# Kernel tuning notes

Hardware: AMD Instinct MI355X
Metric: run time of the kernel (lower is better)

Reference implementation:

```python
import jax, jax.numpy as jnp
import numpy as np
from jax import lax

B, T, H, M, K, Q, P = 32, 128, 256, 1000, 3, 4, 2  # batch, phones, hidden, max_mel_len, kernel, q_out, p_out


def _ln(x, g, b, eps=1e-5):
    mu = jnp.mean(x, -1, keepdims=True)
    var = jnp.mean((x - mu) ** 2, -1, keepdims=True)
    return (x - mu) * lax.rsqrt(var + eps) * g + b


def _forward(x, x_mask, x_dur, params):
    (proj_w, proj_b, conv_w, conv_b, conv_g, conv_beta,
     q_w1, q_b1, q_g, q_beta, q_w2, q_b2,
     p_w1, p_b1, p_g, p_beta, p_w2, p_b2,
     proj1_w, proj1_b, proj2_w, proj2_b, projo_w, projo_b) = params

    valid = (~x_mask).astype(x.dtype)[:, :, None]                      # (B,T,1), 1 = real phone
    # proj -> ConvBlock (shared between the w and c branches; dropout is identity in eval)
    h = x @ proj_w + proj_b                                            # (B,T,H)
    hc = lax.conv_general_dilated((h * valid).transpose(0, 2, 1), conv_w,
                                  (1,), 'SAME',
                                  dimension_numbers=('NCH', 'OIH', 'NCH'))
    hc = hc.transpose(0, 2, 1) + conv_b                                # (B,T,8)
    hc = jax.nn.silu(_ln(hc, conv_g, conv_beta)) * valid               # (B,T,8)

    mel_lens = jnp.minimum(jnp.round(jnp.sum(x_dur, -1)).astype(jnp.int32), M)
    mel_pad = jnp.arange(M)[None, :] >= mel_lens[:, None]              # (B,M) True = padded frame
    mask = x_mask[:, None, :] | mel_pad[:, :, None]                    # (B,M,T)

    e = jnp.cumsum(x_dur, -1)                                          # phone end times
    s = e - x_dur                                                      # phone start times
    t = jnp.arange(1, M + 1, dtype=x.dtype)
    E = jnp.where(mask, 0.0, e[:, None, :] - t[None, :, None])         # (B,M,T)
    S = jnp.where(mask, 0.0, t[None, :, None] - s[:, None, :])         # (B,M,T)

    feat = jnp.concatenate([jnp.broadcast_to(hc[:, None], (B, M, T, 8)),
                            S[..., None], E[..., None]], axis=-1)      # (B,M,T,10)

    # mlp_q scores -> masked softmax over phone axis
    sc = jax.nn.silu(_ln(feat @ q_w1 + q_b1, q_g, q_beta)) @ q_w2 + q_b2   # (B,M,T,Q)
    sc = jnp.where(x_mask[:, None, :, None], -jnp.inf, sc)
    w = jax.nn.softmax(sc, axis=2)
    w = jnp.where(mel_pad[:, :, None, None], 0.0, w)                   # (B,M,T,Q)

    # mlp_p per-(frame,phone) auxiliary features
    c = jax.nn.silu(_ln(feat @ p_w1 + p_b1, p_g, p_beta)) @ p_w2 + p_b2    # (B,M,T,P)

    # dual einsum combine (matches torch permute+view ordering: q-major then feature)
    wh = jnp.einsum('bmnq,bnh->bmqh', w, x).reshape(B, M, Q * H) @ proj1_w + proj1_b
    wc = jnp.einsum('bmnq,bmnp->bmqp', w, c).reshape(B, M, Q * P) @ proj2_w + proj2_b
    o = jnp.where(mel_pad[:, :, None], 0.0, wh + wc) @ projo_w + projo_b   # (B,M,2H)

    mel_mask = jnp.broadcast_to(mel_pad[:, :, None], (B, M, T))
    return o, mel_mask, mel_lens, jnp.transpose(w, (0, 3, 1, 2))


def setup_inputs() -> dict:
    key = jax.random.key(0)
    ks = jax.random.split(key, 16)
    x = jax.random.normal(ks[0], (B, T, H), jnp.float32)
    x_lengths = jax.random.randint(ks[1], (B,), T // 2, T + 1).at[0].set(T)
    x_mask = jnp.arange(T)[None, :] >= x_lengths[:, None]              # True = pad
    x_dur = jax.random.uniform(ks[2], (B, T), jnp.float32, 2.0, 10.0)
    x_dur = x_dur * (~x_mask)
    x_dur = x_dur.at[0].multiply(2.0)  # element 0 total duration > M -> static max_mel_len = M

    def xavier(k, shape):
        return jax.random.normal(k, shape, jnp.float32) * jnp.sqrt(2.0 / (shape[0] + shape[1]))

    return dict(
        x=x, x_mask=x_mask, x_dur=x_dur, x_lengths=x_lengths,
        proj_w=xavier(ks[3], (H, H)), proj_b=jnp.zeros((H,)),
        conv_w=jax.random.normal(ks[4], (8, H, K), jnp.float32) * 0.05, conv_b=jnp.zeros((8,)),
        conv_g=jnp.ones((8,)), conv_beta=jnp.zeros((8,)),
        q_w1=xavier(ks[5], (10, Q)), q_b1=jnp.zeros((Q,)),
        q_g=jnp.ones((Q,)), q_beta=jnp.zeros((Q,)),
        q_w2=xavier(ks[6], (Q, Q)), q_b2=jnp.zeros((Q,)),
        p_w1=xavier(ks[7], (10, P)), p_b1=jnp.zeros((P,)),
        p_g=jnp.ones((P,)), p_beta=jnp.zeros((P,)),
        p_w2=xavier(ks[8], (P, P)), p_b2=jnp.zeros((P,)),
        proj1_w=xavier(ks[9], (H * Q, H)), proj1_b=jnp.zeros((H,)),
        proj2_w=xavier(ks[10], (Q * P, H)), proj2_b=jnp.zeros((H,)),
        projo_w=xavier(ks[11], (H, 2 * H)), projo_b=jnp.zeros((2 * H,)),
    )


def reference(x, x_mask, x_dur, x_lengths,
              proj_w, proj_b, conv_w, conv_b, conv_g, conv_beta,
              q_w1, q_b1, q_g, q_beta, q_w2, q_b2,
              p_w1, p_b1, p_g, p_beta, p_w2, p_b2,
              proj1_w, proj1_b, proj2_w, proj2_b, projo_w, projo_b):
    params = (proj_w, proj_b, conv_w, conv_b, conv_g, conv_beta,
              q_w1, q_b1, q_g, q_beta, q_w2, q_b2,
              p_w1, p_b1, p_g, p_beta, p_w2, p_b2,
              proj1_w, proj1_b, proj2_w, proj2_b, projo_w, projo_b)
    return _forward(x, x_mask, x_dur, params)
```

## Files before the change

kernel.cpp:

```cpp
#include <hip/hip_runtime.h>
#include <math.h>

#define BB 32
#define TT 128
#define HH 256
#define MM 1000

typedef __attribute__((ext_vector_type(8))) short short8;
typedef __attribute__((ext_vector_type(4))) float floatx4;

__device__ inline void fma4(float4& a, const float4 b, float s) {
    a.x += b.x * s; a.y += b.y * s; a.z += b.z * s; a.w += b.w * s;
}

__device__ inline unsigned short f2bf(float f) {
    union { float f; unsigned int u; } c; c.f = f;
    unsigned int u = c.u;
    return (unsigned short)((u + 0x7FFFu + ((u >> 16) & 1u)) >> 16);
}

__device__ inline float bf2f(unsigned short h) {
    union { unsigned int u; float f; } c; c.u = ((unsigned int)h) << 16; return c.f;
}


__global__ __launch_bounds__(256) void kF1(
    const float* __restrict__ x, const float* __restrict__ pw_h_,
    const float* __restrict__ pb_h, float* __restrict__ h,
    const float* __restrict__ p1w, const float* __restrict__ po,
    float* __restrict__ PWpart,
    unsigned short* __restrict__ xh, unsigned short* __restrict__ xl,
    const float* __restrict__ dur, float* __restrict__ e_cum,
    int* __restrict__ ml_i, float* __restrict__ ml_out,
    unsigned short* __restrict__ w_bf) {
    __shared__ __align__(16) float S1[4096];
    int gb = blockIdx.x;
    int tid = threadIdx.x;

    if (gb < 256) {
        float (*xs)[HH] = (float(*)[HH])S1;
        int b = gb >> 3, tt = gb & 7;
        int t0 = tt * 16;
        for (int e = tid; e < 16 * HH; e += 256) {
            int r = e >> 8, i = e & 255;
            xs[r][i] = x[(b * TT + t0 + r) * HH + i];
        }
        __syncthreads();
        int jg = tid & 63, rg = tid >> 6;
        int j4 = jg * 4;
        float4 bias = *(const float4*)(pb_h + j4);
        float4 acc[4];
        #pragma unroll
        for (int ri = 0; ri < 4; ++ri) acc[ri] = bias;
        #pragma unroll 4
        for (int i = 0; i < HH; ++i) {
            float4 wv = *(const float4*)(pw_h_ + i * HH + j4);
            #pragma unroll
// ... 38 lines not shown
        #pragma unroll
        for (int k = 0; k < 4; ++k) {
            unsigned short hv = f2bf(vv[k]);
            hi.us[k] = hv;
            lo.us[k] = f2bf(vv[k] - bf2f(hv));
        }
        *(uint2*)(xh + idx) = hi.u;
        *(uint2*)(xl + idx) = lo.u;
    } else {
        int b = gb - 1792;
        if (tid < 64) {
            #pragma unroll
            for (int q = 0; q < 4; ++q) {
                uint4* dst = (uint4*)(w_bf + (((size_t)(b * 4 + q)) * 1024 + 1000) * 128);
                for (int e = tid; e < 384; e += 64) dst[e] = make_uint4(0, 0, 0, 0);
            }
            if (tid == 0) {
                float run = 0.f;
                const float* d = dur + b * TT;
                float* e = e_cum + b * TT;
                for (int t = 0; t < TT; ++t) { run += d[t]; e[t] = run; }
                int ml = (int)rintf(run);
                if (ml > MM) ml = MM;
                if (ml < 0) ml = 0;
                ml_i[b] = ml;
                ml_out[b] = (float)ml;
            }
        }
    }
}

__global__ __launch_bounds__(256) void kF2(
    const float* __restrict__ h, const float* __restrict__ cw,
    const int* __restrict__ xlen, float* __restrict__ hcpre,
    const float* __restrict__ PWpart,
    unsigned short* __restrict__ pwh, unsigned short* __restrict__ pwl,
    const float* __restrict__ p2w, const float* __restrict__ po,
    const float* __restrict__ p1b, const float* __restrict__ p2b,
    const float* __restrict__ pob,
    float* __restrict__ P2o, float* __restrict__ bvec) {
    __shared__ __align__(16) float S2[10778];
    int gb = blockIdx.x;
    int tid = threadIdx.x;

    if (gb < 256) {
        float (*hs)[257] = (float(*)[257])S2;
        float (*cws)[769] = (float(*)[769])(S2 + 4626);
        int b = gb >> 3, tt = gb & 7;
        int t0 = tt * 16;
        int L = xlen[b];
        for (int e = tid; e < 18 * 256; e += 256) {
            int r = e >> 8, i = e & 255;
            int t = t0 - 1 + r;
            float v = 0.f;
            if (t >= 0 && t < TT && t < L) v = h[((size_t)b * TT + t) * HH + i];
            hs[r][i] = v;
        }
        for (int e = tid; e < 6144; e += 256) {
            int o = e / 768, rem = e - o * 768;
            cws[o][rem] = cw[e];
        }
        __syncthreads();
        if (tid < 128) {
            int o = tid >> 4, tl = tid & 15;
            float acc = 0.f;
            #pragma unroll
            for (int k = 0; k < 3; ++k) {
                const float* wr = &cws[o][k];
                const float* hr = hs[tl + k];
                #pragma unroll 8
                for (int i = 0; i < 256; ++i) acc += hr[i] * wr[i * 3];
            }
            hcpre[((size_t)b * TT + t0 + tl) * 8 + o] = acc;
        }
    } else if (gb < 384) {
        float (*S)[65] = (float(*)[65])S2;
        int blk = gb - 256;
        int nt = blk & 31, ct = blk >> 5;
        int c0 = ct * 64, n0 = nt * 64;
        for (int e = tid; e < 4096; e += 256) {
            int cc = e >> 6, nn = e & 63;
            size_t off = (size_t)(c0 + cc) * 2048 + n0 + nn;
            float v = PWpart[off] + PWpart[524288 + off]
                    + PWpart[2 * 524288 + off] + PWpart[3 * 524288 + off];
            S[cc][nn] = v;
        }
        __syncthreads();
        for (int e = tid; e < 4096; e += 256) {
            int nn = e >> 6, cc = e & 63;
            float v = S[cc][nn];
            unsigned short hv = f2bf(v);
            size_t d = (size_t)(n0 + nn) * 256 + c0 + cc;
            pwh[d] = hv;
            pwl[d] = f2bf(v - bf2f(hv));
        }
    } else {
        for (int j = tid; j < 512; j += 256) {
            float acc[9];
            #pragma unroll
            for (int r = 0; r < 9; ++r) acc[r] = 0.f;
            for (int c = 0; c < HH; ++c) {
                float pv = po[c * 512 + j];
                #pragma unroll
                for (int r = 0; r < 8; ++r) acc[r] += p2w[r * HH + c] * pv;
                acc[8] += (p1b[c] + p2b[c]) * pv;
            }
            #pragma unroll
            for (int r = 0; r < 8; ++r) P2o[r * 512 + j] = acc[r];
            bvec[j] = acc[8] + pob[j];
        }
    }
}

__device__ inline int swzk(int row, int chunk) {
    return row * 32 + ((chunk ^ ((row >> 1) & 3)) << 3);
}

__global__ __launch_bounds__(256) void kF3(
    const unsigned short* __restrict__ xh, const unsigned short* __restrict__ xl,
    const unsigned short* __restrict__ pwh, const unsigned short* __restrict__ pwl,
    unsigned short* __restrict__ A2T,
    const float* __restrict__ hcpre, const float* __restrict__ cb,
    const float* __restrict__ cg, const float* __restrict__ cbeta,
    const float* __restrict__ qw1, const float* __restrict__ qb1,
    const float* __restrict__ pw1, const float* __restrict__ pb1,
    const float* __restrict__ e_cum, const float* __restrict__ dur,
    const int* __restrict__ xlen,
    float* __restrict__ baseq, float* __restrict__ basep) {
    __shared__ __align__(16) unsigned short SM[16384];
    int gblk = blockIdx.x;
    int tid = threadIdx.x;

    if (gblk >= 512) {
        int b = gblk - 512;
        int t = tid;
        if (t < 128) {
            int L = xlen[b];
            float v[8];
            float mu = 0.f;
            #pragma unroll
            for (int o = 0; o < 8; ++o) { v[o] = hcpre[(b * TT + t) * 8 + o] + cb[o]; mu += v[o]; }
            mu *= 0.125f;
            float var = 0.f;
            #pragma unroll
            for (int o = 0; o < 8; ++o) { float d = v[o] - mu; var += d * d; }
            var *= 0.125f;
            float rs = 1.0f / sqrtf(var + 1e-5f);
            float valid = (t < L) ? 1.f : 0.f;
            #pragma unroll
            for (int o = 0; o < 8; ++o) {
                float a = (v[o] - mu) * rs * cg[o] + cbeta[o];
                v[o] = a / (1.f + expf(-a)) * valid;
            }
            float e = e_cum[b * TT + t];
            float s_ = e - dur[b * TT + t];
            #pragma unroll
            for (int j = 0; j < 4; ++j) {
                float acc = qb1[j];
                #pragma unroll
                for (int o = 0; o < 8; ++o) acc += v[o] * qw1[o * 4 + j];
                acc += e * qw1[9 * 4 + j] - s_ * qw1[8 * 4 + j];
                baseq[(b * TT + t) * 4 + j] = acc;
            }
            #pragma unroll
            for (int j = 0; j < 2; ++j) {
                float acc = pb1[j];
                #pragma unroll
                for (int o = 0; o < 8; ++o) acc += v[o] * pw1[o * 2 + j];
                acc += e * pw1[9 * 2 + j] - s_ * pw1[8 * 2 + j];
                basep[(b * TT + t) * 2 + j] = acc;
            }
        }
        return;
    }

    unsigned short* Ah = SM;
    unsigned short* Al = SM + 4096;
    unsigned short* Bh = SM + 8192;
    unsigned short* Bl = SM + 12288;
    int blk = gblk;
    int b = blk >> 4, nt = blk & 15;
    int n0 = nt * 128;
    int lane = tid & 63, wv = tid >> 6;
    int wm = wv & 1, wn = wv >> 1;

    floatx4 acc[16];
    #pragma unroll
    for (int i = 0; i < 16; ++i) acc[i] = (floatx4){0.f, 0.f, 0.f, 0.f};

    int srow = tid >> 1, shalf = tid & 1;
    const unsigned short* gxh = xh + ((size_t)(b * TT + srow) * 256 + shalf * 16);
    const unsigned short* gxl = xl + ((size_t)(b * TT + srow) * 256 + shalf * 16);
    const unsigned short* gph = pwh + ((size_t)(n0 + srow) * 256 + shalf * 16);
    const unsigned short* gpl = pwl + ((size_t)(n0 + srow) * 256 + shalf * 16);
    int wAd0 = swzk(srow, 2 * shalf);
    int wAd1 = swzk(srow, 2 * shalf + 1);

    int ra = wm * 64 + (lane & 15);
    int rb = wn * 64 + (lane & 15);
    int cq = lane >> 4;

    for (int kc = 0; kc < 256; kc += 32) {
        uint4 a0 = *(const uint4*)(gxh + kc);
        uint4 a1 = *(const uint4*)(gxh + kc + 8);
// ... 18 lines not shown
        }
        #pragma unroll
        for (int i = 0; i < 4; ++i)
            #pragma unroll
            for (int j = 0; j < 4; ++j) {
                floatx4 c = acc[i * 4 + j];
                c = __builtin_amdgcn_mfma_f32_16x16x32_bf16(afh[i], bfh[j], c, 0, 0, 0);
                c = __builtin_amdgcn_mfma_f32_16x16x32_bf16(afh[i], bfl[j], c, 0, 0, 0);
                c = __builtin_amdgcn_mfma_f32_16x16x32_bf16(afl[i], bfh[j], c, 0, 0, 0);
                acc[i * 4 + j] = c;
            }
        __syncthreads();
    }

    unsigned short* OT = SM;
    #pragma unroll
    for (int i = 0; i < 4; ++i)
        #pragma unroll
        for (int j = 0; j < 4; ++j) {
            int nloc = wn * 64 + j * 16 + (lane & 15);
            int tb = wm * 64 + i * 16 + ((lane >> 4) << 2);
            union { unsigned short us[4]; uint2 v; } pk;
            #pragma unroll
            for (int r = 0; r < 4; ++r) pk.us[r] = f2bf(acc[i * 4 + j][r]);
            int chunk = tb >> 3, sub = tb & 7;
            *(uint2*)&OT[nloc * 128 + (((chunk ^ (nloc & 15)) << 3) | sub)] = pk.v;
        }
    __syncthreads();
    int q = n0 >> 9, jb = n0 & 511;
    for (int u = tid; u < 2048; u += 256) {
        int nrow = u >> 4, seg = u & 15;
        uint4 v = *(const uint4*)&OT[nrow * 128 + ((seg ^ (nrow & 15)) << 3)];
        *(uint4*)(A2T + (((size_t)(b * 4 + q) * 512) + jb + nrow) * 128 + seg * 8) = v;
    }
}

__global__ __launch_bounds__(256) void k_wsoft(
    const float* __restrict__ baseq, const float* __restrict__ basep,
    const float* __restrict__ qw1, const float* __restrict__ qg,
    const float* __restrict__ qbeta, const float* __restrict__ qw2,
    const float* __restrict__ qb2,
    const float* __restrict__ pw1, const float* __restrict__ pg,
    const float* __restrict__ pbeta, const float* __restrict__ pw2,
    const float* __restrict__ pb2,
    const int* __restrict__ xlen, const int* __restrict__ ml_i,
    float* __restrict__ w_out, float* __restrict__ mm_out,
    float* __restrict__ wc8, unsigned short* __restrict__ w_bf) {
    int blk = blockIdx.x;
    int b = blk / 250;
    int mg = blk - b * 250;
    int wv = threadIdx.x >> 6, lane = threadIdx.x & 63;
    int m = mg * 4 + wv;
    int ml = ml_i[b];
    int t1 = lane, t2 = lane + 64;
    bool pad = (m >= ml);
    size_t mmbase = ((size_t)b * MM + m) * TT;
    mm_out[mmbase + t1] = pad ? 1.f : 0.f;
    mm_out[mmbase + t2] = pad ? 1.f : 0.f;
    if (pad) {
        #pragma unroll
        for (int q = 0; q < 4; ++q) {
            size_t wb = ((size_t)(b * 4 + q) * MM + m) * TT;
            w_out[wb + t1] = 0.f;
            w_out[wb + t2] = 0.f;
            unsigned short* wbq = w_bf + (((size_t)(b * 4 + q)) * 1024 + m) * 128;
            wbq[t1] = 0; wbq[t2] = 0;
        }
        if (lane == 0) {
            #pragma unroll
            for (int r = 0; r < 8; ++r) wc8[((size_t)b * MM + m) * 8 + r] = 0.f;
        }
        return;
    }
    int L = xlen[b];
    float mp1 = (float)(m + 1);
    float dq[4];
    #pragma unroll
    for (int j = 0; j < 4; ++j) dq[j] = mp1 * (qw1[8 * 4 + j] - qw1[9 * 4 + j]);

    float sc1[4], sc2[4];
    float c1v[2], c2v[2];
    #pragma unroll
    for (int half = 0; half < 2; ++half) {
        int t = half ? t2 : t1;
        float* sc = half ? sc2 : sc1;
        float* cv = half ? c2v : c1v;
        if (t < L) {
            float4 bq = *(const float4*)(baseq + ((size_t)b * TT + t) * 4);
            float z[4] = {bq.x + dq[0], bq.y + dq[1], bq.z + dq[2], bq.w + dq[3]};
            float mu = 0.25f * (z[0] + z[1] + z[2] + z[3]);
            float var = 0.f;
            #pragma unroll
            for (int j = 0; j < 4; ++j) { float d = z[j] - mu; var += d * d; }
            var *= 0.25f;
            float rs = 1.f / sqrtf(var + 1e-5f);
            float a[4];
            #pragma unroll
            for (int j = 0; j < 4; ++j) {
                float av = (z[j] - mu) * rs * qg[j] + qbeta[j];
                a[j] = av / (1.f + expf(-av));
            }
            #pragma unroll
            for (int q = 0; q < 4; ++q) {
                float s = qb2[q];
                #pragma unroll
                for (int j = 0; j < 4; ++j) s += a[j] * qw2[j * 4 + q];
                sc[q] = s;
            }
            float z0 = basep[((size_t)b * TT + t) * 2 + 0] + mp1 * (pw1[16] - pw1[18]);
            float z1 = basep[((size_t)b * TT + t) * 2 + 1] + mp1 * (pw1[17] - pw1[19]);
            float pmu = 0.5f * (z0 + z1);
            float d0 = z0 - pmu, d1 = z1 - pmu;
            float pvar = 0.5f * (d0 * d0 + d1 * d1);
            float prs = 1.f / sqrtf(pvar + 1e-5f);
            float a0 = d0 * prs * pg[0] + pbeta[0];
            float a1 = d1 * prs * pg[1] + pbeta[1];
            a0 = a0 / (1.f + expf(-a0));
            a1 = a1 / (1.f + expf(-a1));
            cv[0] = pb2[0] + a0 * pw2[0] + a1 * pw2[2];
            cv[1] = pb2[1] + a0 * pw2[1] + a1 * pw2[3];
        } else {
            sc[0] = sc[1] = sc[2] = sc[3] = -__builtin_inff();
            cv[0] = cv[1] = 0.f;
        }
    }
    float w1[4], w2[4];
    #pragma unroll
    for (int q = 0; q < 4; ++q) {
        float mx = fmaxf(sc1[q], sc2[q]);
        #pragma unroll
        for (int off = 32; off > 0; off >>= 1) mx = fmaxf(mx, __shfl_xor(mx, off, 64));
        float e1 = expf(sc1[q] - mx);
        float e2 = expf(sc2[q] - mx);
        float s = e1 + e2;
        #pragma unroll
        for (int off = 32; off > 0; off >>= 1) s += __shfl_xor(s, off, 64);
        w1[q] = e1 / s;
        w2[q] = e2 / s;
        size_t wb = ((size_t)(b * 4 + q) * MM + m) * TT;
        w_out[wb + t1] = w1[q];
        w_out[wb + t2] = w2[q];
        unsigned short* wbq = w_bf + (((size_t)(b * 4 + q)) * 1024 + m) * 128;
        wbq[t1] = f2bf(w1[q]);
        wbq[t2] = f2bf(w2[q]);
    }
    float red[8];
    #pragma unroll
    for (int r8 = 0; r8 < 8; ++r8) {
        int q = r8 >> 1, p = r8 & 1;
        float v = w1[q] * c1v[p] + w2[q] * c2v[p];
        #pragma unroll
        for (int off = 32; off > 0; off >>= 1) v += __shfl_xor(v, off, 64);
        red[r8] = v;
    }
    if (lane == 0) {
        #pragma unroll
        for (int r8 = 0; r8 < 8; ++r8) wc8[((size_t)b * MM + m) * 8 + r8] = red[r8];
    }
}

__global__ __launch_bounds__(256, 2) void k_main(
    const unsigned short* __restrict__ w_bf, const unsigned short* __restrict__ A2T,
    const float* __restrict__ wc8, const float* __restrict__ P2o,
    const float* __restrict__ bvec, const float* __restrict__ pob,
    const int* __restrict__ ml_i, float* __restrict__ o_out) {
    __shared__ __align__(16) unsigned short Asm[2][128 * 40];
    __shared__ __align__(16) unsigned short Bsm[2][128 * 40];
    int wgid = blockIdx.x;
    int blk = (wgid & 7) * 128 + (wgid >> 3);
    int nt = blk & 3, mt = (blk >> 2) & 7, b = blk >> 5;
    int m0 = mt * 128, n0 = nt * 128;
    int tid = threadIdx.x;
    int ml = ml_i[b];

    if (m0 >= ml) {
        float* pb_s = (float*)&Asm[0][0];
        if (tid < 128) pb_s[tid] = pob[n0 + tid];
        __syncthreads();
        int col4 = (tid & 31) * 4;
        float4 pv = *(const float4*)&pb_s[col4];
        for (int r = tid >> 5; r < 128; r += 8) {
            int m = m0 + r;
            if (m < MM)
                *(float4*)(o_out + ((size_t)b * MM + m) * 512 + n0 + col4) = pv;
        }
        return;
    }

    int lane = tid & 63, wv = tid >> 6;
    int wm = wv & 1, wn = wv >> 1;
// ... 109 lines not shown
                              void* d_out, int out_size, void* d_ws, size_t ws_size,
                              hipStream_t stream) {
    (void)in_sizes; (void)n_in; (void)out_size; (void)ws_size;
    const float* x      = (const float*)d_in[0];
    const float* dur    = (const float*)d_in[2];
    const int*   xlen   = (const int*)d_in[3];
    const float* proj_w = (const float*)d_in[4];
    const float* proj_b = (const float*)d_in[5];
    const float* conv_w = (const float*)d_in[6];
    const float* conv_b = (const float*)d_in[7];
    const float* conv_g = (const float*)d_in[8];
    const float* conv_be= (const float*)d_in[9];
    const float* q_w1   = (const float*)d_in[10];
    const float* q_b1   = (const float*)d_in[11];
    const float* q_g    = (const float*)d_in[12];
    const float* q_be   = (const float*)d_in[13];
    const float* q_w2   = (const float*)d_in[14];
    const float* q_b2   = (const float*)d_in[15];
    const float* p_w1   = (const float*)d_in[16];
    const float* p_b1   = (const float*)d_in[17];
    const float* p_g    = (const float*)d_in[18];
    const float* p_be   = (const float*)d_in[19];
    const float* p_w2   = (const float*)d_in[20];
    const float* p_b2   = (const float*)d_in[21];
    const float* p1w    = (const float*)d_in[22];
    const float* p1b    = (const float*)d_in[23];
    const float* p2w    = (const float*)d_in[24];
    const float* p2b    = (const float*)d_in[25];
    const float* pow_   = (const float*)d_in[26];
    const float* pob    = (const float*)d_in[27];

    float* ws    = (float*)d_ws;
    float* e_cum = ws + 0;
    float* hcpre = ws + 4096;
    float* baseq = ws + 36864;
    float* basep = ws + 53248;
    float* h     = ws + 61440;
    unsigned short* pw_h = (unsigned short*)(ws + 1110016);
    unsigned short* pw_l = (unsigned short*)(ws + 1372160);
    unsigned short* A2T = (unsigned short*)(ws + 1634304);
    float* wc8   = ws + 5828608;
    float* P2o   = ws + 6084608;
    float* bvec  = ws + 6088704;
    int*   ml_i  = (int*)(ws + 6089216);
    float* PWpart= ws + 6090752;
    unsigned short* w_bf = (unsigned short*)(ws + 8187904);
    unsigned short* x_hi = (unsigned short*)(ws + 16576512);
    unsigned short* x_lo = (unsigned short*)(ws + 17100800);

    float* o_out  = (float*)d_out;
    float* mm_out = o_out + 16384000;
    float* ml_out = o_out + 20480000;
    float* w_out  = o_out + 20480032;

    kF1<<<dim3(1824), dim3(256), 0, stream>>>(x, proj_w, proj_b, h,
                                              p1w, pow_, PWpart,
                                              x_hi, x_lo,
                                              dur, e_cum, ml_i, ml_out, w_bf);
    kF2<<<dim3(385), dim3(256), 0, stream>>>(h, conv_w, xlen, hcpre,
                                             PWpart, pw_h, pw_l,
                                             p2w, pow_, p1b, p2b, pob, P2o, bvec);
    kF3<<<dim3(544), dim3(256), 0, stream>>>(x_hi, x_lo, pw_h, pw_l, A2T,
                                             hcpre, conv_b, conv_g, conv_be,
                                             q_w1, q_b1, p_w1, p_b1,
                                             e_cum, dur, xlen, baseq, basep);
    k_wsoft<<<dim3(BB * 250), dim3(256), 0, stream>>>(baseq, basep,
                                                      q_w1, q_g, q_be, q_w2, q_b2,
                                                      p_w1, p_g, p_be, p_w2, p_b2,
                                                      xlen, ml_i, w_out, mm_out, wc8, w_bf);
    k_main<<<dim3(BB * 32), dim3(256), 0, stream>>>(w_bf, A2T, wc8, P2o, bvec,
                                                    pob, ml_i, o_out);
}
```

Measured before the change: 373.4 us.

## Fuse softmax-weight kernel into kF3 and recompute per-phone base features inline

Merges k_wsoft into kF3 as extra blocks (grid grows from 544 to 8512), removing one kernel launch and the baseq/basep intermediate buffers. Each softmax block now recomputes the conv layernorm/SiLU and first-layer projections per phone instead of reading precomputed values. This trades redundant arithmetic (recomputed per mel frame, about 1000x per phone) for one fewer launch and the ability to overlap with the GEMM blocks of kF3.

```diff
diff --git a/kernel.cpp b/kernel.cpp
--- a/kernel.cpp
+++ b/kernel.cpp
@@ -23,6 +23,49 @@
     union { unsigned int u; float f; } c; c.u = ((unsigned int)h) << 16; return c.f;
 }
 
+
+__device__ inline void base_eval(
+    const float* __restrict__ hcpre, const float* __restrict__ cb,
+    const float* __restrict__ cg, const float* __restrict__ cbeta,
+    const float* __restrict__ qw1, const float* __restrict__ qb1,
+    const float* __restrict__ pw1, const float* __restrict__ pb1,
+    const float* __restrict__ e_cum, const float* __restrict__ dur,
+    int b, int t, int L, float bq[4], float bp[2]) {
+    float v[8];
+    float mu = 0.f;
+    #pragma unroll
+    for (int o = 0; o < 8; ++o) { v[o] = hcpre[(b * TT + t) * 8 + o] + cb[o]; mu += v[o]; }
+    mu *= 0.125f;
+    float var = 0.f;
+    #pragma unroll
+    for (int o = 0; o < 8; ++o) { float d = v[o] - mu; var += d * d; }
+    var *= 0.125f;
+    float rs = 1.0f / sqrtf(var + 1e-5f);
+    float valid = (t < L) ? 1.f : 0.f;
+    #pragma unroll
+    for (int o = 0; o < 8; ++o) {
+        float a = (v[o] - mu) * rs * cg[o] + cbeta[o];
+        v[o] = a / (1.f + expf(-a)) * valid;
+    }
+    float e = e_cum[b * TT + t];
+    float s_ = e - dur[b * TT + t];
+    #pragma unroll
+    for (int j = 0; j < 4; ++j) {
+        float acc = qb1[j];
+        #pragma unroll
+        for (int o = 0; o < 8; ++o) acc += v[o] * qw1[o * 4 + j];
+        acc += e * qw1[9 * 4 + j] - s_ * qw1[8 * 4 + j];
+        bq[j] = acc;
+    }
+    #pragma unroll
+    for (int j = 0; j < 2; ++j) {
+        float acc = pb1[j];
+        #pragma unroll
+        for (int o = 0; o < 8; ++o) acc += v[o] * pw1[o * 2 + j];
+        acc += e * pw1[9 * 2 + j] - s_ * pw1[8 * 2 + j];
+        bp[j] = acc;
+    }
+}
 
 __global__ __launch_bounds__(256) void kF1(
     const float* __restrict__ x, const float* __restrict__ pw_h_,
@@ -221,50 +264,130 @@
     const float* __restrict__ pw1, const float* __restrict__ pb1,
     const float* __restrict__ e_cum, const float* __restrict__ dur,
     const int* __restrict__ xlen,
-    float* __restrict__ baseq, float* __restrict__ basep) {
+    const float* __restrict__ qg, const float* __restrict__ qbeta,
+    const float* __restrict__ qw2, const float* __restrict__ qb2,
+    const float* __restrict__ pg, const float* __restrict__ pbeta,
+    const float* __restrict__ pw2, const float* __restrict__ pb2,
+    const int* __restrict__ ml_i,
+    float* __restrict__ w_out, float* __restrict__ mm_out,
+    float* __restrict__ wc8, unsigned short* __restrict__ w_bf) {
     __shared__ __align__(16) unsigned short SM[16384];
     int gblk = blockIdx.x;
     int tid = threadIdx.x;
 
     if (gblk >= 512) {
-        int b = gblk - 512;
-        int t = tid;
-        if (t < 128) {
-            int L = xlen[b];
-            float v[8];
-            float mu = 0.f;
-            #pragma unroll
-            for (int o = 0; o < 8; ++o) { v[o] = hcpre[(b * TT + t) * 8 + o] + cb[o]; mu += v[o]; }
-            mu *= 0.125f;
-            float var = 0.f;
-            #pragma unroll
-            for (int o = 0; o < 8; ++o) { float d = v[o] - mu; var += d * d; }
-            var *= 0.125f;
-            float rs = 1.0f / sqrtf(var + 1e-5f);
-            float valid = (t < L) ? 1.f : 0.f;
-            #pragma unroll
-            for (int o = 0; o < 8; ++o) {
-                float a = (v[o] - mu) * rs * cg[o] + cbeta[o];
-                v[o] = a / (1.f + expf(-a)) * valid;
-            }
-            float e = e_cum[b * TT + t];
-            float s_ = e - dur[b * TT + t];
-            #pragma unroll
-            for (int j = 0; j < 4; ++j) {
-                float acc = qb1[j];
+        int blk = gblk - 512;
+        int b = blk / 250;
+        int mg = blk - b * 250;
+        int wv = tid >> 6, lane = tid & 63;
+        int m = mg * 4 + wv;
+        int ml = ml_i[b];
+        int t1 = lane, t2 = lane + 64;
+        bool pad = (m >= ml);
+        size_t mmbase = ((size_t)b * MM + m) * TT;
+        mm_out[mmbase + t1] = pad ? 1.f : 0.f;
+        mm_out[mmbase + t2] = pad ? 1.f : 0.f;
+        if (pad) {
+            #pragma unroll
+            for (int q = 0; q < 4; ++q) {
+                size_t wb = ((size_t)(b * 4 + q) * MM + m) * TT;
+                w_out[wb + t1] = 0.f;
+                w_out[wb + t2] = 0.f;
+                unsigned short* wbq = w_bf + (((size_t)(b * 4 + q)) * 1024 + m) * 128;
+                wbq[t1] = 0; wbq[t2] = 0;
+            }
+            if (lane == 0) {
                 #pragma unroll
-                for (int o = 0; o < 8; ++o) acc += v[o] * qw1[o * 4 + j];
-                acc += e * qw1[9 * 4 + j] - s_ * qw1[8 * 4 + j];
-                baseq[(b * TT + t) * 4 + j] = acc;
-            }
-            #pragma unroll
-            for (int j = 0; j < 2; ++j) {
-                float acc = pb1[j];
+                for (int r = 0; r < 8; ++r) wc8[((size_t)b * MM + m) * 8 + r] = 0.f;
+            }
+            return;
+        }
+        int L = xlen[b];
+        float mp1 = (float)(m + 1);
+        float dq[4];
+        #pragma unroll
+        for (int j = 0; j < 4; ++j) dq[j] = mp1 * (qw1[8 * 4 + j] - qw1[9 * 4 + j]);
+
+        float sc1[4], sc2[4];
+        float c1v[2], c2v[2];
+        #pragma unroll
+        for (int half = 0; half < 2; ++half) {
+            int t = half ? t2 : t1;
+            float* sc = half ? sc2 : sc1;
+            float* cv = half ? c2v : c1v;
+            if (t < L) {
+                float bq[4], bp[2];
+                base_eval(hcpre, cb, cg, cbeta, qw1, qb1, pw1, pb1,
+                          e_cum, dur, b, t, L, bq, bp);
+                float z[4] = {bq[0] + dq[0], bq[1] + dq[1], bq[2] + dq[2], bq[3] + dq[3]};
+                float mu = 0.25f * (z[0] + z[1] + z[2] + z[3]);
+                float var = 0.f;
                 #pragma unroll
-                for (int o = 0; o < 8; ++o) acc += v[o] * pw1[o * 2 + j];
-                acc += e * pw1[9 * 2 + j] - s_ * pw1[8 * 2 + j];
-                basep[(b * TT + t) * 2 + j] = acc;
-            }
+                for (int j = 0; j < 4; ++j) { float d = z[j] - mu; var += d * d; }
+                var *= 0.25f;
+                float rs = 1.f / sqrtf(var + 1e-5f);
+                float a[4];
+                #pragma unroll
+                for (int j = 0; j < 4; ++j) {
+                    float av = (z[j] - mu) * rs * qg[j] + qbeta[j];
+                    a[j] = av / (1.f + expf(-av));
+                }
+                #pragma unroll
+                for (int q = 0; q < 4; ++q) {
+                    float s = qb2[q];
+                    #pragma unroll
+                    for (int j = 0; j < 4; ++j) s += a[j] * qw2[j * 4 + q];
+                    sc[q] = s;
+                }
+                float z0 = bp[0] + mp1 * (pw1[16] - pw1[18]);
+                float z1 = bp[1] + mp1 * (pw1[17] - pw1[19]);
+                float pmu = 0.5f * (z0 + z1);
+                float d0 = z0 - pmu, d1 = z1 - pmu;
+                float pvar = 0.5f * (d0 * d0 + d1 * d1);
+                float prs = 1.f / sqrtf(pvar + 1e-5f);
+                float a0 = d0 * prs * pg[0] + pbeta[0];
+                float a1 = d1 * prs * pg[1] + pbeta[1];
+                a0 = a0 / (1.f + expf(-a0));
+                a1 = a1 / (1.f + expf(-a1));
+                cv[0] = pb2[0] + a0 * pw2[0] + a1 * pw2[2];
+                cv[1] = pb2[1] + a0 * pw2[1] + a1 * pw2[3];
+            } else {
+                sc[0] = sc[1] = sc[2] = sc[3] = -__builtin_inff();
+                cv[0] = cv[1] = 0.f;
+            }
+        }
+        float w1[4], w2[4];
+        #pragma unroll
+        for (int q = 0; q < 4; ++q) {
+            float mx = fmaxf(sc1[q], sc2[q]);
+            #pragma unroll
+            for (int off = 32; off > 0; off >>= 1) mx = fmaxf(mx, __shfl_xor(mx, off, 64));
+            float e1 = expf(sc1[q] - mx);
+            float e2 = expf(sc2[q] - mx);
+            float s = e1 + e2;
+            #pragma unroll
+            for (int off = 32; off > 0; off >>= 1) s += __shfl_xor(s, off, 64);
+            w1[q] = e1 / s;
+            w2[q] = e2 / s;
+            size_t wb = ((size_t)(b * 4 + q) * MM + m) * TT;
+            w_out[wb + t1] = w1[q];
+            w_out[wb + t2] = w2[q];
+            unsigned short* wbq = w_bf + (((size_t)(b * 4 + q)) * 1024 + m) * 128;
+            wbq[t1] = f2bf(w1[q]);
+            wbq[t2] = f2bf(w2[q]);
+        }
+        float red[8];
+        #pragma unroll
+        for (int r8 = 0; r8 < 8; ++r8) {
+            int q = r8 >> 1, p = r8 & 1;
+            float v = w1[q] * c1v[p] + w2[q] * c2v[p];
+            #pragma unroll
+            for (int off = 32; off > 0; off >>= 1) v += __shfl_xor(v, off, 64);
+            red[r8] = v;
+        }
+        if (lane == 0) {
+            #pragma unroll
+            for (int r8 = 0; r8 < 8; ++r8) wc8[((size_t)b * MM + m) * 8 + r8] = red[r8];
         }
         return;
     }
@@ -349,130 +472,6 @@
         int nrow = u >> 4, seg = u & 15;
         uint4 v = *(const uint4*)&OT[nrow * 128 + ((seg ^ (nrow & 15)) << 3)];
         *(uint4*)(A2T + (((size_t)(b * 4 + q) * 512) + jb + nrow) * 128 + seg * 8) = v;
-    }
-}
-
-__global__ __launch_bounds__(256) void k_wsoft(
-    const float* __restrict__ baseq, const float* __restrict__ basep,
-    const float* __restrict__ qw1, const float* __restrict__ qg,
-    const float* __restrict__ qbeta, const float* __restrict__ qw2,
-    const float* __restrict__ qb2,
-    const float* __restrict__ pw1, const float* __restrict__ pg,
-    const float* __restrict__ pbeta, const float* __restrict__ pw2,
-    const float* __restrict__ pb2,
-    const int* __restrict__ xlen, const int* __restrict__ ml_i,
-    float* __restrict__ w_out, float* __restrict__ mm_out,
-    float* __restrict__ wc8, unsigned short* __restrict__ w_bf) {
-    int blk = blockIdx.x;
-    int b = blk / 250;
-    int mg = blk - b * 250;
-    int wv = threadIdx.x >> 6, lane = threadIdx.x & 63;
-    int m = mg * 4 + wv;
-    int ml = ml_i[b];
-    int t1 = lane, t2 = lane + 64;
-    bool pad = (m >= ml);
-    size_t mmbase = ((size_t)b * MM + m) * TT;
-    mm_out[mmbase + t1] = pad ? 1.f : 0.f;
-    mm_out[mmbase + t2] = pad ? 1.f : 0.f;
-    if (pad) {
-        #pragma unroll
-        for (int q = 0; q < 4; ++q) {
-            size_t wb = ((size_t)(b * 4 + q) * MM + m) * TT;
-            w_out[wb + t1] = 0.f;
-            w_out[wb + t2] = 0.f;
-            unsigned short* wbq = w_bf + (((size_t)(b * 4 + q)) * 1024 + m) * 128;
-            wbq[t1] = 0; wbq[t2] = 0;
-        }
-        if (lane == 0) {
-            #pragma unroll
-            for (int r = 0; r < 8; ++r) wc8[((size_t)b * MM + m) * 8 + r] = 0.f;
-        }
-        return;
-    }
-    int L = xlen[b];
-    float mp1 = (float)(m + 1);
-    float dq[4];
-    #pragma unroll
-    for (int j = 0; j < 4; ++j) dq[j] = mp1 * (qw1[8 * 4 + j] - qw1[9 * 4 + j]);
-
-    float sc1[4], sc2[4];
-    float c1v[2], c2v[2];
-    #pragma unroll
-    for (int half = 0; half < 2; ++half) {
-        int t = half ? t2 : t1;
-        float* sc = half ? sc2 : sc1;
-        float* cv = half ? c2v : c1v;
-        if (t < L) {
-            float4 bq = *(const float4*)(baseq + ((size_t)b * TT + t) * 4);
-            float z[4] = {bq.x + dq[0], bq.y + dq[1], bq.z + dq[2], bq.w + dq[3]};
-            float mu = 0.25f * (z[0] + z[1] + z[2] + z[3]);
-            float var = 0.f;
-            #pragma unroll
-            for (int j = 0; j < 4; ++j) { float d = z[j] - mu; var += d * d; }
-            var *= 0.25f;
-            float rs = 1.f / sqrtf(var + 1e-5f);
-            float a[4];
-            #pragma unroll
-            for (int j = 0; j < 4; ++j) {
-                float av = (z[j] - mu) * rs * qg[j] + qbeta[j];
-                a[j] = av / (1.f + expf(-av));
-            }
-            #pragma unroll
-            for (int q = 0; q < 4; ++q) {
-                float s = qb2[q];
-                #pragma unroll
-                for (int j = 0; j < 4; ++j) s += a[j] * qw2[j * 4 + q];
-                sc[q] = s;
-            }
-            float z0 = basep[((size_t)b * TT + t) * 2 + 0] + mp1 * (pw1[16] - pw1[18]);
-            float z1 = basep[((size_t)b * TT + t) * 2 + 1] + mp1 * (pw1[17] - pw1[19]);
-            float pmu = 0.5f * (z0 + z1);
-            float d0 = z0 - pmu, d1 = z1 - pmu;
-            float pvar = 0.5f * (d0 * d0 + d1 * d1);
-            float prs = 1.f / sqrtf(pvar + 1e-5f);
-            float a0 = d0 * prs * pg[0] + pbeta[0];
-            float a1 = d1 * prs * pg[1] + pbeta[1];
-            a0 = a0 / (1.f + expf(-a0));
-            a1 = a1 / (1.f + expf(-a1));
-            cv[0] = pb2[0] + a0 * pw2[0] + a1 * pw2[2];
-            cv[1] = pb2[1] + a0 * pw2[1] + a1 * pw2[3];
-        } else {
-            sc[0] = sc[1] = sc[2] = sc[3] = -__builtin_inff();
-            cv[0] = cv[1] = 0.f;
-        }
-    }
-    float w1[4], w2[4];
-    #pragma unroll
-    for (int q = 0; q < 4; ++q) {
-        float mx = fmaxf(sc1[q], sc2[q]);
-        #pragma unroll
-        for (int off = 32; off > 0; off >>= 1) mx = fmaxf(mx, __shfl_xor(mx, off, 64));
-        float e1 = expf(sc1[q] - mx);
-        float e2 = expf(sc2[q] - mx);
-        float s = e1 + e2;
-        #pragma unroll
-        for (int off = 32; off > 0; off >>= 1) s += __shfl_xor(s, off, 64);
-        w1[q] = e1 / s;
-        w2[q] = e2 / s;
-        size_t wb = ((size_t)(b * 4 + q) * MM + m) * TT;
-        w_out[wb + t1] = w1[q];
-        w_out[wb + t2] = w2[q];
-        unsigned short* wbq = w_bf + (((size_t)(b * 4 + q)) * 1024 + m) * 128;
-        wbq[t1] = f2bf(w1[q]);
-        wbq[t2] = f2bf(w2[q]);
-    }
-    float red[8];
-    #pragma unroll
-    for (int r8 = 0; r8 < 8; ++r8) {
-        int q = r8 >> 1, p = r8 & 1;
-        float v = w1[q] * c1v[p] + w2[q] * c2v[p];
-        #pragma unroll
-        for (int off = 32; off > 0; off >>= 1) v += __shfl_xor(v, off, 64);
-        red[r8] = v;
-    }
-    if (lane == 0) {
-        #pragma unroll
-        for (int r8 = 0; r8 < 8; ++r8) wc8[((size_t)b * MM + m) * 8 + r8] = red[r8];
     }
 }
 
@@ -649,8 +648,6 @@
     float* ws    = (float*)d_ws;
     float* e_cum = ws + 0;
     float* hcpre = ws + 4096;
-    float* baseq = ws + 36864;
-    float* basep = ws + 53248;
     float* h     = ws + 61440;
     unsigned short* pw_h = (unsigned short*)(ws + 1110016);
     unsigned short* pw_l = (unsigned short*)(ws + 1372160);
@@ -676,14 +673,13 @@
     kF2<<<dim3(385), dim3(256), 0, stream>>>(h, conv_w, xlen, hcpre,
                                              PWpart, pw_h, pw_l,
                                              p2w, pow_, p1b, p2b, pob, P2o, bvec);
-    kF3<<<dim3(544), dim3(256), 0, stream>>>(x_hi, x_lo, pw_h, pw_l, A2T,
-                                             hcpre, conv_b, conv_g, conv_be,
-                                             q_w1, q_b1, p_w1, p_b1,
-                                             e_cum, dur, xlen, baseq, basep);
-    k_wsoft<<<dim3(BB * 250), dim3(256), 0, stream>>>(baseq, basep,
-                                                      q_w1, q_g, q_be, q_w2, q_b2,
-                                                      p_w1, p_g, p_be, p_w2, p_b2,
-                                                      xlen, ml_i, w_out, mm_out, wc8, w_bf);
+    kF3<<<dim3(8512), dim3(256), 0, stream>>>(x_hi, x_lo, pw_h, pw_l, A2T,
+                                              hcpre, conv_b, conv_g, conv_be,
+                                              q_w1, q_b1, p_w1, p_b1,
+                                              e_cum, dur, xlen,
+                                              q_g, q_be, q_w2, q_b2,
+                                              p_g, p_be, p_w2, p_b2,
+                                              ml_i, w_out, mm_out, wc8, w_bf);
     k_main<<<dim3(BB * 32), dim3(256), 0, stream>>>(w_bf, A2T, wc8, P2o, bvec,
                                                     pob, ml_i, o_out);
 }
```

New measurement: 408.3 us. 1.09x slower.

## Fuse conv LN/SiLU epilogue into kF2 and merge softmax kernel into kF3

Applied to the files above, without the earlier changes.

The conv-block LayerNorm/SiLU and the base q/p projections now run inside the kF2 conv blocks through shared memory, so the hcpre round trip through global memory goes away. The separate k_wsoft softmax kernel is folded into kF3 as extra blocks (grid grows from 544 to 8512), which removes one kernel launch and lets the softmax work overlap the A2T GEMM blocks. In exchange, kF3's shared-memory footprint now applies to the many lightweight softmax blocks, which may limit their occupancy.

```diff
diff --git a/kernel.cpp b/kernel.cpp
--- a/kernel.cpp
+++ b/kernel.cpp
@@ -127,20 +127,27 @@
 
 __global__ __launch_bounds__(256) void kF2(
     const float* __restrict__ h, const float* __restrict__ cw,
-    const int* __restrict__ xlen, float* __restrict__ hcpre,
+    const int* __restrict__ xlen,
     const float* __restrict__ PWpart,
     unsigned short* __restrict__ pwh, unsigned short* __restrict__ pwl,
     const float* __restrict__ p2w, const float* __restrict__ po,
     const float* __restrict__ p1b, const float* __restrict__ p2b,
     const float* __restrict__ pob,
-    float* __restrict__ P2o, float* __restrict__ bvec) {
-    __shared__ __align__(16) float S2[10778];
+    float* __restrict__ P2o, float* __restrict__ bvec,
+    const float* __restrict__ cb, const float* __restrict__ cg,
+    const float* __restrict__ cbeta,
+    const float* __restrict__ qw1, const float* __restrict__ qb1,
+    const float* __restrict__ pw1, const float* __restrict__ pb1,
+    const float* __restrict__ e_cum, const float* __restrict__ dur,
+    float* __restrict__ baseq, float* __restrict__ basep) {
+    __shared__ __align__(16) float S2[10906];
     int gb = blockIdx.x;
     int tid = threadIdx.x;
 
     if (gb < 256) {
         float (*hs)[257] = (float(*)[257])S2;
         float (*cws)[769] = (float(*)[769])(S2 + 4626);
+        float (*hc)[8] = (float(*)[8])(S2 + 10778);
         int b = gb >> 3, tt = gb & 7;
         int t0 = tt * 16;
         int L = xlen[b];
@@ -166,7 +173,45 @@
                 #pragma unroll 8
                 for (int i = 0; i < 256; ++i) acc += hr[i] * wr[i * 3];
             }
-            hcpre[((size_t)b * TT + t0 + tl) * 8 + o] = acc;
+            hc[tl][o] = acc;
+        }
+        __syncthreads();
+        if (tid < 16) {
+            int t = t0 + tid;
+            float v[8];
+            float mu = 0.f;
+            #pragma unroll
+            for (int o = 0; o < 8; ++o) { v[o] = hc[tid][o] + cb[o]; mu += v[o]; }
+            mu *= 0.125f;
+            float var = 0.f;
+            #pragma unroll
+            for (int o = 0; o < 8; ++o) { float d = v[o] - mu; var += d * d; }
+            var *= 0.125f;
+            float rs = 1.0f / sqrtf(var + 1e-5f);
+            float valid = (t < L) ? 1.f : 0.f;
+            #pragma unroll
+            for (int o = 0; o < 8; ++o) {
+                float a = (v[o] - mu) * rs * cg[o] + cbeta[o];
+                v[o] = a / (1.f + expf(-a)) * valid;
+            }
+            float e = e_cum[b * TT + t];
+            float s_ = e - dur[b * TT + t];
+            #pragma unroll
+            for (int j = 0; j < 4; ++j) {
+                float acc = qb1[j];
+                #pragma unroll
+                for (int o = 0; o < 8; ++o) acc += v[o] * qw1[o * 4 + j];
+                acc += e * qw1[9 * 4 + j] - s_ * qw1[8 * 4 + j];
+                baseq[(b * TT + t) * 4 + j] = acc;
+            }
+            #pragma unroll
+            for (int j = 0; j < 2; ++j) {
+                float acc = pb1[j];
+                #pragma unroll
+                for (int o = 0; o < 8; ++o) acc += v[o] * pw1[o * 2 + j];
+                acc += e * pw1[9 * 2 + j] - s_ * pw1[8 * 2 + j];
+                basep[(b * TT + t) * 2 + j] = acc;
+            }
         }
     } else if (gb < 384) {
         float (*S)[65] = (float(*)[65])S2;
@@ -215,56 +260,131 @@
     const unsigned short* __restrict__ xh, const unsigned short* __restrict__ xl,
     const unsigned short* __restrict__ pwh, const unsigned short* __restrict__ pwl,
     unsigned short* __restrict__ A2T,
-    const float* __restrict__ hcpre, const float* __restrict__ cb,
-    const float* __restrict__ cg, const float* __restrict__ cbeta,
-    const float* __restrict__ qw1, const float* __restrict__ qb1,
-    const float* __restrict__ pw1, const float* __restrict__ pb1,
-    const float* __restrict__ e_cum, const float* __restrict__ dur,
-    const int* __restrict__ xlen,
-    float* __restrict__ baseq, float* __restrict__ basep) {
+    const float* __restrict__ baseq, const float* __restrict__ basep,
+    const float* __restrict__ qw1, const float* __restrict__ qg,
+    const float* __restrict__ qbeta, const float* __restrict__ qw2,
+    const float* __restrict__ qb2,
+    const float* __restrict__ pw1, const float* __restrict__ pg,
+    const float* __restrict__ pbeta, const float* __restrict__ pw2,
+    const float* __restrict__ pb2,
+    const int* __restrict__ xlen, const int* __restrict__ ml_i,
+    float* __restrict__ w_out, float* __restrict__ mm_out,
+    float* __restrict__ wc8, unsigned short* __restrict__ w_bf) {
     __shared__ __align__(16) unsigned short SM[16384];
     int gblk = blockIdx.x;
     int tid = threadIdx.x;
 
     if (gblk >= 512) {
-        int b = gblk - 512;
-        int t = tid;
-        if (t < 128) {
-            int L = xlen[b];
-            float v[8];
-            float mu = 0.f;
-            #pragma unroll
-            for (int o = 0; o < 8; ++o) { v[o] = hcpre[(b * TT + t) * 8 + o] + cb[o]; mu += v[o]; }
-            mu *= 0.125f;
-            float var = 0.f;
-            #pragma unroll
-            for (int o = 0; o < 8; ++o) { float d = v[o] - mu; var += d * d; }
-            var *= 0.125f;
-            float rs = 1.0f / sqrtf(var + 1e-5f);
-            float valid = (t < L) ? 1.f : 0.f;
-            #pragma unroll
-            for (int o = 0; o < 8; ++o) {
-                float a = (v[o] - mu) * rs * cg[o] + cbeta[o];
-                v[o] = a / (1.f + expf(-a)) * valid;
-            }
-            float e = e_cum[b * TT + t];
-            float s_ = e - dur[b * TT + t];
-            #pragma unroll
-            for (int j = 0; j < 4; ++j) {
-                float acc = qb1[j];
-                #pragma unroll
-                for (int o = 0; o < 8; ++o) acc += v[o] * qw1[o * 4 + j];
-                acc += e * qw1[9 * 4 + j] - s_ * qw1[8 * 4 + j];
-                baseq[(b * TT + t) * 4 + j] = acc;
-            }
-            #pragma unroll
-            for (int j = 0; j < 2; ++j) {
-                float acc = pb1[j];
-                #pragma unroll
-                for (int o = 0; o < 8; ++o) acc += v[o] * pw1[o * 2 + j];
-                acc += e * pw1[9 * 2 + j] - s_ * pw1[8 * 2 + j];
-                basep[(b * TT + t) * 2 + j] = acc;
-            }
+        int blk = gblk - 512;
+        int b = blk / 250;
+        int mg = blk - b * 250;
+        int wv = tid >> 6, lane = tid & 63;
+        int m = mg * 4 + wv;
+        int ml = ml_i[b];
+        int t1 = lane, t2 = lane + 64;
+        bool pad = (m >= ml);
+        size_t mmbase = ((size_t)b * MM + m) * TT;
+        mm_out[mmbase + t1] = pad ? 1.f : 0.f;
+        mm_out[mmbase + t2] = pad ? 1.f : 0.f;
+        if (pad) {
+            #pragma unroll
+            for (int q = 0; q < 4; ++q) {
+                size_t wb = ((size_t)(b * 4 + q) * MM + m) * TT;
+                w_out[wb + t1] = 0.f;
+                w_out[wb + t2] = 0.f;
+                unsigned short* wbq = w_bf + (((size_t)(b * 4 + q)) * 1024 + m) * 128;
+                wbq[t1] = 0; wbq[t2] = 0;
+            }
+            if (lane == 0) {
+                #pragma unroll
+                for (int r = 0; r < 8; ++r) wc8[((size_t)b * MM + m) * 8 + r] = 0.f;
+            }
+            return;
+        }
+        int L = xlen[b];
+        float mp1 = (float)(m + 1);
+        float dq[4];
+        #pragma unroll
+        for (int j = 0; j < 4; ++j) dq[j] = mp1 * (qw1[8 * 4 + j] - qw1[9 * 4 + j]);
+
+        float sc1[4], sc2[4];
+        float c1v[2], c2v[2];
+        #pragma unroll
+        for (int half = 0; half < 2; ++half) {
+            int t = half ? t2 : t1;
+            float* sc = half ? sc2 : sc1;
+            float* cv = half ? c2v : c1v;
+            if (t < L) {
+                float4 bq = *(const float4*)(baseq + ((size_t)b * TT + t) * 4);
+                float z[4] = {bq.x + dq[0], bq.y + dq[1], bq.z + dq[2], bq.w + dq[3]};
+                float mu = 0.25f * (z[0] + z[1] + z[2] + z[3]);
+                float var = 0.f;
+                #pragma unroll
+                for (int j = 0; j < 4; ++j) { float d = z[j] - mu; var += d * d; }
+                var *= 0.25f;
+                float rs = 1.f / sqrtf(var + 1e-5f);
+                float a[4];
+                #pragma unroll
+                for (int j = 0; j < 4; ++j) {
+                    float av = (z[j] - mu) * rs * qg[j] + qbeta[j];
+                    a[j] = av / (1.f + expf(-av));
+                }
+                #pragma unroll
+                for (int q = 0; q < 4; ++q) {
+                    float s = qb2[q];
+                    #pragma unroll
+                    for (int j = 0; j < 4; ++j) s += a[j] * qw2[j * 4 + q];
+                    sc[q] = s;
+                }
+                float z0 = basep[((size_t)b * TT + t) * 2 + 0] + mp1 * (pw1[16] - pw1[18]);
+                float z1 = basep[((size_t)b * TT + t) * 2 + 1] + mp1 * (pw1[17] - pw1[19]);
+                float pmu = 0.5f * (z0 + z1);
+                float d0 = z0 - pmu, d1 = z1 - pmu;
+                float pvar = 0.5f * (d0 * d0 + d1 * d1);
+                float prs = 1.f / sqrtf(pvar + 1e-5f);
+                float a0 = d0 * prs * pg[0] + pbeta[0];
+                float a1 = d1 * prs * pg[1] + pbeta[1];
+                a0 = a0 / (1.f + expf(-a0));
+                a1 = a1 / (1.f + expf(-a1));
+                cv[0] = pb2[0] + a0 * pw2[0] + a1 * pw2[2];
+                cv[1] = pb2[1] + a0 * pw2[1] + a1 * pw2[3];
+            } else {
+                sc[0] = sc[1] = sc[2] = sc[3] = -__builtin_inff();
+                cv[0] = cv[1] = 0.f;
+            }
+        }
+        float w1[4], w2[4];
+        #pragma unroll
+        for (int q = 0; q < 4; ++q) {
+            float mx = fmaxf(sc1[q], sc2[q]);
+            #pragma unroll
+            for (int off = 32; off > 0; off >>= 1) mx = fmaxf(mx, __shfl_xor(mx, off, 64));
+            float e1 = expf(sc1[q] - mx);
+            float e2 = expf(sc2[q] - mx);
+            float s = e1 + e2;
+            #pragma unroll
+            for (int off = 32; off > 0; off >>= 1) s += __shfl_xor(s, off, 64);
+            w1[q] = e1 / s;
+            w2[q] = e2 / s;
+            size_t wb = ((size_t)(b * 4 + q) * MM + m) * TT;
+            w_out[wb + t1] = w1[q];
+            w_out[wb + t2] = w2[q];
+            unsigned short* wbq = w_bf + (((size_t)(b * 4 + q)) * 1024 + m) * 128;
+            wbq[t1] = f2bf(w1[q]);
+            wbq[t2] = f2bf(w2[q]);
+        }
+        float red[8];
+        #pragma unroll
+        for (int r8 = 0; r8 < 8; ++r8) {
+            int q = r8 >> 1, p = r8 & 1;
+            float v = w1[q] * c1v[p] + w2[q] * c2v[p];
+            #pragma unroll
+            for (int off = 32; off > 0; off >>= 1) v += __shfl_xor(v, off, 64);
+            red[r8] = v;
+        }
+        if (lane == 0) {
+            #pragma unroll
+            for (int r8 = 0; r8 < 8; ++r8) wc8[((size_t)b * MM + m) * 8 + r8] = red[r8];
         }
         return;
     }
@@ -349,130 +469,6 @@
         int nrow = u >> 4, seg = u & 15;
         uint4 v = *(const uint4*)&OT[nrow * 128 + ((seg ^ (nrow & 15)) << 3)];
         *(uint4*)(A2T + (((size_t)(b * 4 + q) * 512) + jb + nrow) * 128 + seg * 8) = v;
-    }
-}
-
-__global__ __launch_bounds__(256) void k_wsoft(
-    const float* __restrict__ baseq, const float* __restrict__ basep,
-    const float* __restrict__ qw1, const float* __restrict__ qg,
-    const float* __restrict__ qbeta, const float* __restrict__ qw2,
-    const float* __restrict__ qb2,
-    const float* __restrict__ pw1, const float* __restrict__ pg,
-    const float* __restrict__ pbeta, const float* __restrict__ pw2,
-    const float* __restrict__ pb2,
-    const int* __restrict__ xlen, const int* __restrict__ ml_i,
-    float* __restrict__ w_out, float* __restrict__ mm_out,
-    float* __restrict__ wc8, unsigned short* __restrict__ w_bf) {
-    int blk = blockIdx.x;
-    int b = blk / 250;
-    int mg = blk - b * 250;
-    int wv = threadIdx.x >> 6, lane = threadIdx.x & 63;
-    int m = mg * 4 + wv;
-    int ml = ml_i[b];
-    int t1 = lane, t2 = lane + 64;
-    bool pad = (m >= ml);
-    size_t mmbase = ((size_t)b * MM + m) * TT;
-    mm_out[mmbase + t1] = pad ? 1.f : 0.f;
-    mm_out[mmbase + t2] = pad ? 1.f : 0.f;
-    if (pad) {
-        #pragma unroll
-        for (int q = 0; q < 4; ++q) {
-            size_t wb = ((size_t)(b * 4 + q) * MM + m) * TT;
-            w_out[wb + t1] = 0.f;
-            w_out[wb + t2] = 0.f;
-            unsigned short* wbq = w_bf + (((size_t)(b * 4 + q)) * 1024 + m) * 128;
-            wbq[t1] = 0; wbq[t2] = 0;
-        }
-        if (lane == 0) {
-            #pragma unroll
-            for (int r = 0; r < 8; ++r) wc8[((size_t)b * MM + m) * 8 + r] = 0.f;
-        }
-        return;
-    }
-    int L = xlen[b];
-    float mp1 = (float)(m + 1);
-    float dq[4];
-    #pragma unroll
-    for (int j = 0; j < 4; ++j) dq[j] = mp1 * (qw1[8 * 4 + j] - qw1[9 * 4 + j]);
-
-    float sc1[4], sc2[4];
-    float c1v[2], c2v[2];
-    #pragma unroll
-    for (int half = 0; half < 2; ++half) {
-        int t = half ? t2 : t1;
-        float* sc = half ? sc2 : sc1;
-        float* cv = half ? c2v : c1v;
-        if (t < L) {
-            float4 bq = *(const float4*)(baseq + ((size_t)b * TT + t) * 4);
-            float z[4] = {bq.x + dq[0], bq.y + dq[1], bq.z + dq[2], bq.w + dq[3]};
-            float mu = 0.25f * (z[0] + z[1] + z[2] + z[3]);
-            float var = 0.f;
-            #pragma unroll
-            for (int j = 0; j < 4; ++j) { float d = z[j] - mu; var += d * d; }
-            var *= 0.25f;
-            float rs = 1.f / sqrtf(var + 1e-5f);
-            float a[4];
-            #pragma unroll
-            for (int j = 0; j < 4; ++j) {
-                float av = (z[j] - mu) * rs * qg[j] + qbeta[j];
-                a[j] = av / (1.f + expf(-av));
-            }
-            #pragma unroll
-            for (int q = 0; q < 4; ++q) {
-                float s = qb2[q];
-                #pragma unroll
-                for (int j = 0; j < 4; ++j) s += a[j] * qw2[j * 4 + q];
-                sc[q] = s;
-            }
-            float z0 = basep[((size_t)b * TT + t) * 2 + 0] + mp1 * (pw1[16] - pw1[18]);
-            float z1 = basep[((size_t)b * TT + t) * 2 + 1] + mp1 * (pw1[17] - pw1[19]);
-            float pmu = 0.5f * (z0 + z1);
-            float d0 = z0 - pmu, d1 = z1 - pmu;
-            float pvar = 0.5f * (d0 * d0 + d1 * d1);
-            float prs = 1.f / sqrtf(pvar + 1e-5f);
-            float a0 = d0 * prs * pg[0] + pbeta[0];
-            float a1 = d1 * prs * pg[1] + pbeta[1];
-            a0 = a0 / (1.f + expf(-a0));
-            a1 = a1 / (1.f + expf(-a1));
-            cv[0] = pb2[0] + a0 * pw2[0] + a1 * pw2[2];
-            cv[1] = pb2[1] + a0 * pw2[1] + a1 * pw2[3];
-        } else {
-            sc[0] = sc[1] = sc[2] = sc[3] = -__builtin_inff();
-            cv[0] = cv[1] = 0.f;
-        }
-    }
-    float w1[4], w2[4];
-    #pragma unroll
-    for (int q = 0; q < 4; ++q) {
-        float mx = fmaxf(sc1[q], sc2[q]);
-        #pragma unroll
-        for (int off = 32; off > 0; off >>= 1) mx = fmaxf(mx, __shfl_xor(mx, off, 64));
-        float e1 = expf(sc1[q] - mx);
-        float e2 = expf(sc2[q] - mx);
-        float s = e1 + e2;
-        #pragma unroll
-        for (int off = 32; off > 0; off >>= 1) s += __shfl_xor(s, off, 64);
-        w1[q] = e1 / s;
-        w2[q] = e2 / s;
-        size_t wb = ((size_t)(b * 4 + q) * MM + m) * TT;
-        w_out[wb + t1] = w1[q];
-        w_out[wb + t2] = w2[q];
-        unsigned short* wbq = w_bf + (((size_t)(b * 4 + q)) * 1024 + m) * 128;
-        wbq[t1] = f2bf(w1[q]);
-        wbq[t2] = f2bf(w2[q]);
-    }
-    float red[8];
-    #pragma unroll
-    for (int r8 = 0; r8 < 8; ++r8) {
-        int q = r8 >> 1, p = r8 & 1;
-        float v = w1[q] * c1v[p] + w2[q] * c2v[p];
-        #pragma unroll
-        for (int off = 32; off > 0; off >>= 1) v += __shfl_xor(v, off, 64);
-        red[r8] = v;
-    }
-    if (lane == 0) {
-        #pragma unroll
-        for (int r8 = 0; r8 < 8; ++r8) wc8[((size_t)b * MM + m) * 8 + r8] = red[r8];
     }
 }
 
@@ -648,7 +644,6 @@
 
     float* ws    = (float*)d_ws;
     float* e_cum = ws + 0;
-    float* hcpre = ws + 4096;
     float* baseq = ws + 36864;
     float* basep = ws + 53248;
     float* h     = ws + 61440;
@@ -673,17 +668,17 @@
                                               p1w, pow_, PWpart,
                                               x_hi, x_lo,
                                               dur, e_cum, ml_i, ml_out, w_bf);
-    kF2<<<dim3(385), dim3(256), 0, stream>>>(h, conv_w, xlen, hcpre,
+    kF2<<<dim3(385), dim3(256), 0, stream>>>(h, conv_w, xlen,
                                              PWpart, pw_h, pw_l,
-                                             p2w, pow_, p1b, p2b, pob, P2o, bvec);
-    kF3<<<dim3(544), dim3(256), 0, stream>>>(x_hi, x_lo, pw_h, pw_l, A2T,
-                                             hcpre, conv_b, conv_g, conv_be,
+                                             p2w, pow_, p1b, p2b, pob, P2o, bvec,
+                                             conv_b, conv_g, conv_be,
                                              q_w1, q_b1, p_w1, p_b1,
-                                             e_cum, dur, xlen, baseq, basep);
-    k_wsoft<<<dim3(BB * 250), dim3(256), 0, stream>>>(baseq, basep,
-                                                      q_w1, q_g, q_be, q_w2, q_b2,
-                                                      p_w1, p_g, p_be, p_w2, p_b2,
-                                                      xlen, ml_i, w_out, mm_out, wc8, w_bf);
+                                             e_cum, dur, baseq, basep);
+    kF3<<<dim3(8512), dim3(256), 0, stream>>>(x_hi, x_lo, pw_h, pw_l, A2T,
+                                              baseq, basep,
+                                              q_w1, q_g, q_be, q_w2, q_b2,
+                                              p_w1, p_g, p_be, p_w2, p_b2,
+                                              xlen, ml_i, w_out, mm_out, wc8, w_bf);
     k_main<<<dim3(BB * 32), dim3(256), 0, stream>>>(w_bf, A2T, wc8, P2o, bvec,
                                                     pob, ml_i, o_out);
 }
```

After: 372.8 us. No clear change (-0.2%).
